# Kernel tuning notes

Hardware: AMD Instinct MI355X
Metric: run time of the kernel (lower is better)

The kernel has to match this reference:

```python
import jax, jax.numpy as jnp
import numpy as np

B, C, L = 32, 64, 2048
FREQ = L // 2 + 1            # 1025
BAND_SIZES = [341, 341, 343]  # freq//3, freq//3, remainder


def setup_inputs() -> dict:
    key = jax.random.key(0)
    k = jax.random.split(key, 6)
    X = jax.random.normal(k[0], (B, C, L), dtype=jnp.float32)
    A0 = jax.random.normal(k[1], (BAND_SIZES[0], BAND_SIZES[0]), dtype=jnp.float32)
    A1 = jax.random.normal(k[2], (BAND_SIZES[1], BAND_SIZES[1]), dtype=jnp.float32)
    A2 = jax.random.normal(k[3], (BAND_SIZES[2], BAND_SIZES[2]), dtype=jnp.float32)
    fusion_weights = jnp.ones((3,), dtype=jnp.float32)
    # Gumbel(0,1) noise for the 2-way gumbel-softmax over each (b, i, j) entry
    gumbel_noise = jax.random.gumbel(k[4], (B, C, C, 2), dtype=jnp.float32)
    return {"X": X, "A0": A0, "A1": A1, "A2": A2,
            "fusion_weights": fusion_weights, "gumbel_noise": gumbel_noise}


def _band_dist(band, A):
    # band: (b, c, s), A: (s, s). dist[b,i,j] = ||A (band_i - band_j)||^2
    # Gram trick: ||y_i - y_j||^2 = q_i + q_j - 2 y_i . y_j, y = band @ A^T
    Y = jnp.einsum('ds,bcs->bcd', A, band)          # (b, c, s)
    G = jnp.einsum('bid,bjd->bij', Y, Y)            # (b, c, c)
    q = jnp.einsum('bid,bid->bi', Y, Y)             # (b, c)
    dist = q[:, :, None] + q[:, None, :] - 2.0 * G
    return jnp.maximum(dist, 0.0)                   # guard fp round-off


def reference(X, A0, A1, A2, fusion_weights, gumbel_noise):
    XF = jnp.abs(jnp.fft.rfft(X, axis=-1))          # (b, c, FREQ)
    s0, s1, s2 = BAND_SIZES
    bands = (XF[..., :s0], XF[..., s0:s0 + s1], XF[..., s0 + s1:])
    As = (A0, A1, A2)
    dists = jnp.stack([_band_dist(b_, A_) for b_, A_ in zip(bands, As)], axis=-1)  # (b,c,c,3)
    w = jax.nn.softmax(fusion_weights)
    dist = jnp.einsum('bijk,k->bij', dists, w)      # (b, c, c)

    exp_dist = 1.0 / (dist + 1e-10)
    eye = jnp.eye(C, dtype=exp_dist.dtype)
    mask = 1.0 - eye
    exp_dist = exp_dist * mask
    exp_max = jax.lax.stop_gradient(jnp.max(exp_dist, axis=-1, keepdims=True))
    p = exp_dist / exp_max
    p = (p * mask + eye) * 0.99                     # probs in (0, 0.99]

    # Bernoulli via 2-class gumbel-softmax (hard, tau=1, straight-through)
    logits = jnp.stack([jnp.log(p / (1.0 - p)), jnp.log((1.0 - p) / p)], axis=-1)  # (b,c,c,2)
    y = logits + gumbel_noise
    y_soft = jax.nn.softmax(y, axis=-1)
    y_hard = jax.nn.one_hot(jnp.argmax(y, axis=-1), 2, dtype=y_soft.dtype)
    sample = (y_hard - jax.lax.stop_gradient(y_soft) + y_soft)[..., 0]  # (b,c,c)
    return sample[:, None, :, :]                    # (b, 1, c, c)
```

## Files before the change

kernel.cpp:

```cpp
#include <hip/hip_runtime.h>
#include <math.h>

#define Bn 32
#define Cn 64
#define Ln 2048
#define NFREQ 1025
#define S0c 341
#define S1c 341
#define S2c 343

#define PI_D 3.14159265358979323846

typedef double v4d __attribute__((ext_vector_type(4)));

#define PADIX(i) ((i) + ((i) >> 4))

__global__ void k_twiddle(double2* __restrict__ tw) {
    int t = blockIdx.x * blockDim.x + threadIdx.x;
    if (t < 2048) {
        double ang = -2.0 * PI_D * (double)t / 2048.0;
        double s, c;
        sincos(ang, &s, &c);
        tw[t] = make_double2(c, s);
    }
}

__device__ __forceinline__ int rev4_10(unsigned x) {
    unsigned t = __brev(x) >> 22;
    return (int)(((t & 0x155u) << 1) | ((t >> 1) & 0x155u));
}

__global__ __launch_bounds__(256) void k_fft(const float* __restrict__ X,
                                             const double2* __restrict__ tw,
                                             float* __restrict__ XF) {
    __shared__ double re[1088];
    __shared__ double im[1088];
    int row = blockIdx.x;
    int tid = threadIdx.x;
    const float2* xr = (const float2*)(X + (size_t)row * Ln);
    {
        int k = tid;
        float2 v0 = xr[k];
        float2 v1 = xr[k + 256];
        float2 v2 = xr[k + 512];
        float2 v3 = xr[k + 768];
        double ar = (double)v0.x, ai = (double)v0.y;
        double br = (double)v1.x, bi = (double)v1.y;
        double cr = (double)v2.x, ci = (double)v2.y;
        double dr = (double)v3.x, di = (double)v3.y;
        double2 w1 = tw[2 * k];
        double2 w2 = tw[4 * k];
        double2 w3 = tw[6 * k];
        double t0r = ar + cr, t0i = ai + ci;
        double t1r = ar - cr, t1i = ai - ci;
        double t2r = br + dr, t2i = bi + di;
        double t3r = br - dr, t3i = bi - di;
        int i0 = PADIX(k), i1 = PADIX(k + 256), i2 = PADIX(k + 512), i3 = PADIX(k + 768);
        re[i0] = t0r + t2r; im[i0] = t0i + t2i;
        double u1r = t1r + t3i, u1i = t1i - t3r;
        re[i1] = u1r * w1.x - u1i * w1.y; im[i1] = u1r * w1.y + u1i * w1.x;
        double u2r = t0r - t2r, u2i = t0i - t2i;
        re[i2] = u2r * w2.x - u2i * w2.y; im[i2] = u2r * w2.y + u2i * w2.x;
        double u3r = t1r - t3i, u3i = t1i + t3r;
        re[i3] = u3r * w3.x - u3i * w3.y; im[i3] = u3r * w3.y + u3i * w3.x;
    }
    __syncthreads();
    #pragma unroll
    for (int s = 1; s < 5; ++s) {
        int log2Q = 8 - 2 * s;
        int Q = 1 << log2Q;
        int k = tid & (Q - 1);
        int g = tid >> log2Q;
        int base = (g << (log2Q + 2)) + k;
        int i0 = PADIX(base), i1 = PADIX(base + Q), i2 = PADIX(base + 2 * Q), i3 = PADIX(base + 3 * Q);
        double ar = re[i0], ai = im[i0];
        double br = re[i1], bi = im[i1];
        double cr = re[i2], ci = im[i2];
        double dr = re[i3], di = im[i3];
        int step = 2 << (2 * s);
        double2 w1 = tw[k * step];
        double2 w2 = tw[2 * k * step];
        double2 w3 = tw[3 * k * step];
        double t0r = ar + cr, t0i = ai + ci;
        double t1r = ar - cr, t1i = ai - ci;
        double t2r = br + dr, t2i = bi + di;
        double t3r = br - dr, t3i = bi - di;
        re[i0] = t0r + t2r; im[i0] = t0i + t2i;
        double u1r = t1r + t3i, u1i = t1i - t3r;
        re[i1] = u1r * w1.x - u1i * w1.y; im[i1] = u1r * w1.y + u1i * w1.x;
        double u2r = t0r - t2r, u2i = t0i - t2i;
        re[i2] = u2r * w2.x - u2i * w2.y; im[i2] = u2r * w2.y + u2i * w2.x;
        double u3r = t1r - t3i, u3i = t1i + t3r;
        re[i3] = u3r * w3.x - u3i * w3.y; im[i3] = u3r * w3.y + u3i * w3.x;
        __syncthreads();
    }
    float* out = XF + (size_t)row * NFREQ;
    for (int k = tid; k <= 1024; k += 256) {
        double Xr, Xi;
        if (k == 0)        { Xr = re[0] + im[0]; Xi = 0.0; }
        else if (k == 1024){ Xr = re[0] - im[0]; Xi = 0.0; }
        else {
            int rv  = PADIX(rev4_10((unsigned)k));
            int rv2 = PADIX(rev4_10((unsigned)(1024 - k)));
            double Zr = re[rv],  Zi = im[rv];
            double Wr = re[rv2], Wi = im[rv2];
            double Er = 0.5 * (Zr + Wr), Ei = 0.5 * (Zi - Wi);
            double Or = 0.5 * (Zi + Wi), Oi = -0.5 * (Zr - Wr);
            double2 t = tw[k];
            Xr = Er + t.x * Or - t.y * Oi;
            Xi = Ei + t.x * Oi + t.y * Or;
        }
        out[k] = (float)sqrt(Xr * Xr + Xi * Xi);
    }
}

__global__ __launch_bounds__(256) void k_gemm(const float* __restrict__ XF,
                                              const float* __restrict__ A0,
                                              const float* __restrict__ A1,
                                              const float* __restrict__ A2,
                                              double* __restrict__ Y) {
    const int Sarr[3] = {S0c, S1c, S2c};
    const int Oarr[3] = {0, S0c, S0c + S1c};
    int bz = blockIdx.z;
    int z = bz >> 2, q = bz & 3;
    const float* A = (z == 0) ? A0 : ((z == 1) ? A1 : A2);
    int S = Sarr[z], O = Oarr[z];
    int qm = q >> 1, qn = q & 1;

    __shared__ float sX[32][66];
    __shared__ float sA[32][66];
    int r0 = blockIdx.x * 64 + qm * 32;
    int d0 = blockIdx.y * 64 + qn * 32;
    int tid = threadIdx.x;
    int lane = tid & 63, w = tid >> 6;
    int lm = (w >> 1) * 16, ln = (w & 1) * 16;
    int fm = lane & 15, kq = lane >> 4;
    int kl = tid & 63, rl = tid >> 6;

    v4d zero = {0.0, 0.0, 0.0, 0.0};
    double aval = (double)fm;
    v4d calR = __builtin_amdgcn_mfma_f64_16x16x4f64(aval, 1.0, zero, 0, 0, 0);
    v4d calC = __builtin_amdgcn_mfma_f64_16x16x4f64(1.0, aval, zero, 0, 0, 0);
    int rIdx[4], cIdx[4];
    #pragma unroll
    for (int i = 0; i < 4; ++i) {
        rIdx[i] = (int)(calR[i] * 0.25);
        cIdx[i] = (int)(calC[i] * 0.25);
    }

    auto load_tile = [&](int st, float* px, float* pa) {
        int ss = st * 64 + kl;
        bool sv = ss < S;
        #pragma unroll
        for (int i = 0; i < 8; ++i)
            px[i] = sv ? XF[(size_t)(r0 + rl + 4 * i) * NFREQ + O + ss] : 0.0f;
        #pragma unroll
        for (int j = 0; j < 8; ++j) {
            int d = d0 + rl + 4 * j;
            pa[j] = (sv && d < S) ? A[(size_t)d * S + ss] : 0.0f;
        }
    };

    v4d acc = zero;
    float px[8], pa[8];
    load_tile(0, px, pa);
    const int nsteps = 6;
    for (int st = 0; st < nsteps; ++st) {
        __syncthreads();
        #pragma unroll
        for (int i = 0; i < 8; ++i) sX[rl + 4 * i][kl] = px[i];
        #pragma unroll
        for (int j = 0; j < 8; ++j) sA[rl + 4 * j][kl] = pa[j];
        __syncthreads();
        if (st + 1 < nsteps) load_tile(st + 1, px, pa);
        #pragma unroll
        for (int t = 0; t < 16; ++t) {
            int k = 4 * t + kq;
            double a = (double)sX[lm + fm][k];
            double b = (double)sA[ln + fm][k];
            acc = __builtin_amdgcn_mfma_f64_16x16x4f64(a, b, acc, 0, 0, 0);
        }
    }
    #pragma unroll
    for (int i = 0; i < 4; ++i) {
        int row = r0 + lm + rIdx[i];
        int d = d0 + ln + cIdx[i];
        if (d < S) Y[(size_t)row * NFREQ + O + d] = acc[i];
    }
}

__global__ __launch_bounds__(256) void k_dist(const double* __restrict__ Y,
                                              const float* __restrict__ fw,
                                              double* __restrict__ part) {
    __shared__ double sY[64][34];
    int b = blockIdx.x;
    int chunk = blockIdx.y;
    int dlo = chunk * 128;
    int dhi = (chunk == 7) ? NFREQ : dlo + 128;
    int tid = threadIdx.x;
    int lane = tid & 63, w = tid >> 6;
    int wm = (w >> 1) * 32, wn = (w & 1) * 32;
    int fm = lane & 15, kq = lane >> 4;
    int kl = tid & 31, rl = tid >> 5;

    double f0 = (double)fw[0], f1 = (double)fw[1], f2 = (double)fw[2];
    double m = fmax(f0, fmax(f1, f2));
    double e0 = exp(f0 - m), e1 = exp(f1 - m), e2 = exp(f2 - m);
    double esum = e0 + e1 + e2;
    double sw0 = sqrt(e0 / esum), sw1 = sqrt(e1 / esum), sw2 = sqrt(e2 / esum);

    v4d zero = {0.0, 0.0, 0.0, 0.0};
    double aval = (double)fm;
    v4d calR = __builtin_amdgcn_mfma_f64_16x16x4f64(aval, 1.0, zero, 0, 0, 0);
    v4d calC = __builtin_amdgcn_mfma_f64_16x16x4f64(1.0, aval, zero, 0, 0, 0);
    int rIdx[4], cIdx[4];
    #pragma unroll
    for (int i = 0; i < 4; ++i) {
        rIdx[i] = (int)(calR[i] * 0.25);
        cIdx[i] = (int)(calC[i] * 0.25);
    }

    const double* Yb = Y + (size_t)b * Cn * NFREQ;
    auto load_tile = [&](int k0, double* py) {
        int d = dlo + k0 + kl;
        bool dv = d < dhi;
        double sw = dv ? ((d < S0c) ? sw0 : ((d < S0c + S1c) ? sw1 : sw2)) : 0.0;
        #pragma unroll
        for (int i = 0; i < 8; ++i)
            py[i] = dv ? Yb[(size_t)(rl + 8 * i) * NFREQ + d] * sw : 0.0;
    };

    v4d acc00 = zero, acc01 = zero, acc10 = zero, acc11 = zero;
    double py[8];
    load_tile(0, py);
    int nsteps = (dhi - dlo + 31) / 32;
    for (int st = 0; st < nsteps; ++st) {
        __syncthreads();
        #pragma unroll
        for (int i = 0; i < 8; ++i) sY[rl + 8 * i][kl] = py[i];
        __syncthreads();
        if (st + 1 < nsteps) load_tile((st + 1) * 32, py);
        #pragma unroll
        for (int t = 0; t < 8; ++t) {
            int k = 4 * t + kq;
            double a0 = sY[wm + fm][k];
            double a1 = sY[wm + 16 + fm][k];
            double b0 = sY[wn + fm][k];
            double b1 = sY[wn + 16 + fm][k];
            acc00 = __builtin_amdgcn_mfma_f64_16x16x4f64(a0, b0, acc00, 0, 0, 0);
            acc01 = __builtin_amdgcn_mfma_f64_16x16x4f64(a0, b1, acc01, 0, 0, 0);
            acc10 = __builtin_amdgcn_mfma_f64_16x16x4f64(a1, b0, acc10, 0, 0, 0);
            acc11 = __builtin_amdgcn_mfma_f64_16x16x4f64(a1, b1, acc11, 0, 0, 0);
        }
    }
    double* pb = part + (((size_t)b * 8 + chunk) << 12);
    #pragma unroll
    for (int i = 0; i < 4; ++i) {
        int rowA = wm + rIdx[i], rowB = rowA + 16;
        int cA = wn + cIdx[i], cB = cA + 16;
        pb[rowA * 64 + cA] = acc00[i];
        pb[rowA * 64 + cB] = acc01[i];
        pb[rowB * 64 + cA] = acc10[i];
        pb[rowB * 64 + cB] = acc11[i];
    }
}

__global__ __launch_bounds__(256) void k_decide(const double* __restrict__ part,
                                                const float* __restrict__ gum,
                                                float* __restrict__ out) {
    __shared__ double sQ[64];
    int b = blockIdx.x;
    int tid = threadIdx.x;
    const double* pb = part + (((size_t)b * 8) << 12);
    if (tid < 64) {
        double q = 0.0;
        #pragma unroll
        for (int c = 0; c < 8; ++c) q += pb[((size_t)c << 12) + tid * 65];
        sQ[tid] = q;
    }
    __syncthreads();
    int i = blockIdx.y * 4 + (tid >> 6);
    int j = tid & 63;
    double g = 0.0;
    #pragma unroll
    for (int c = 0; c < 8; ++c) g += pb[((size_t)c << 12) + i * 64 + j];
    double dist = fmax(sQ[i] + sQ[j] - 2.0 * g, 0.0);
    double e = (i == j) ? 0.0 : 1.0 / (dist + 1e-10);
    double emax = e;
    #pragma unroll
    for (int off = 32; off; off >>= 1)
        emax = fmax(emax, __shfl_xor(emax, off, 64));
    double p = (i == j) ? 0.99 : (e / emax) * 0.99;
    double l0 = log(p / (1.0 - p));
    double l1 = log((1.0 - p) / p);
    int idx = i * 64 + j;
    const float* gb = gum + (size_t)b * 8192;
    double y0 = l0 + (double)gb[2 * idx];
    double y1 = l1 + (double)gb[2 * idx + 1];
    out[(size_t)b * 4096 + idx] = (y0 >= y1) ? 1.0f : 0.0f;
}

extern "C" void kernel_launch(void* const* d_in, const int* in_sizes, int n_in,
                              void* d_out, int out_size, void* d_ws, size_t ws_size,
                              hipStream_t stream) {
    const float* X  = (const float*)d_in[0];
    const float* A0 = (const float*)d_in[1];
    const float* A1 = (const float*)d_in[2];
    const float* A2 = (const float*)d_in[3];
    const float* fw = (const float*)d_in[4];
    const float* gm = (const float*)d_in[5];
    float* out = (float*)d_out;

    char* ws = (char*)d_ws;
    double2* tw  = (double2*)(ws);
    float*   XF  = (float*)(ws + 32768);
    double*  Y   = (double*)(ws + 8429568);
    double*  part = (double*)(ws + 32768);

    k_twiddle<<<8, 256, 0, stream>>>(tw);
    k_fft<<<Bn * Cn, 256, 0, stream>>>(X, tw, XF);
    k_gemm<<<dim3(32, 6, 12), 256, 0, stream>>>(XF, A0, A1, A2, Y);
    k_dist<<<dim3(Bn, 8), 256, 0, stream>>>(Y, fw, part);
    k_decide<<<dim3(Bn, 16), 256, 0, stream>>>(part, gm, out);
}
```

Before: 161.8 us.

## Batch two FFT rows per block and shrink GEMM K-tile with dual accumulators

The FFT kernel now handles two rows per block, so twiddle loads and index math are shared across both rows and half as many blocks are launched. The GEMM kernel drops its K-tile from 64 to 32 and sizes the loop count per band (11 steps instead of a fixed 6×64), which removes padded zero work. It also splits the MFMA chain into two accumulators to break the dependency between successive MFMAs. In exchange the FFT uses twice the shared memory per block, the GEMM has more sync steps, and the FFT grid has fewer blocks.

```diff
diff --git a/kernel.cpp b/kernel.cpp
--- a/kernel.cpp
+++ b/kernel.cpp
@@ -33,36 +33,39 @@
 __global__ __launch_bounds__(256) void k_fft(const float* __restrict__ X,
                                              const double2* __restrict__ tw,
                                              float* __restrict__ XF) {
-    __shared__ double re[1088];
-    __shared__ double im[1088];
-    int row = blockIdx.x;
+    __shared__ double re[2][1088];
+    __shared__ double im[2][1088];
+    int row0 = blockIdx.x * 2;
     int tid = threadIdx.x;
-    const float2* xr = (const float2*)(X + (size_t)row * Ln);
     {
         int k = tid;
-        float2 v0 = xr[k];
-        float2 v1 = xr[k + 256];
-        float2 v2 = xr[k + 512];
-        float2 v3 = xr[k + 768];
-        double ar = (double)v0.x, ai = (double)v0.y;
-        double br = (double)v1.x, bi = (double)v1.y;
-        double cr = (double)v2.x, ci = (double)v2.y;
-        double dr = (double)v3.x, di = (double)v3.y;
         double2 w1 = tw[2 * k];
         double2 w2 = tw[4 * k];
         double2 w3 = tw[6 * k];
-        double t0r = ar + cr, t0i = ai + ci;
-        double t1r = ar - cr, t1i = ai - ci;
-        double t2r = br + dr, t2i = bi + di;
-        double t3r = br - dr, t3i = bi - di;
         int i0 = PADIX(k), i1 = PADIX(k + 256), i2 = PADIX(k + 512), i3 = PADIX(k + 768);
-        re[i0] = t0r + t2r; im[i0] = t0i + t2i;
-        double u1r = t1r + t3i, u1i = t1i - t3r;
-        re[i1] = u1r * w1.x - u1i * w1.y; im[i1] = u1r * w1.y + u1i * w1.x;
-        double u2r = t0r - t2r, u2i = t0i - t2i;
-        re[i2] = u2r * w2.x - u2i * w2.y; im[i2] = u2r * w2.y + u2i * w2.x;
-        double u3r = t1r - t3i, u3i = t1i + t3r;
-        re[i3] = u3r * w3.x - u3i * w3.y; im[i3] = u3r * w3.y + u3i * w3.x;
+        #pragma unroll
+        for (int r = 0; r < 2; ++r) {
+            const float2* xr = (const float2*)(X + (size_t)(row0 + r) * Ln);
+            float2 v0 = xr[k];
+            float2 v1 = xr[k + 256];
+            float2 v2 = xr[k + 512];
+            float2 v3 = xr[k + 768];
+            double ar = (double)v0.x, ai = (double)v0.y;
+            double br = (double)v1.x, bi = (double)v1.y;
+            double cr = (double)v2.x, ci = (double)v2.y;
+            double dr = (double)v3.x, di = (double)v3.y;
+            double t0r = ar + cr, t0i = ai + ci;
+            double t1r = ar - cr, t1i = ai - ci;
+            double t2r = br + dr, t2i = bi + di;
+            double t3r = br - dr, t3i = bi - di;
+            re[r][i0] = t0r + t2r; im[r][i0] = t0i + t2i;
+            double u1r = t1r + t3i, u1i = t1i - t3r;
+            re[r][i1] = u1r * w1.x - u1i * w1.y; im[r][i1] = u1r * w1.y + u1i * w1.x;
+            double u2r = t0r - t2r, u2i = t0i - t2i;
+            re[r][i2] = u2r * w2.x - u2i * w2.y; im[r][i2] = u2r * w2.y + u2i * w2.x;
+            double u3r = t1r - t3i, u3i = t1i + t3r;
+            re[r][i3] = u3r * w3.x - u3i * w3.y; im[r][i3] = u3r * w3.y + u3i * w3.x;
+        }
     }
     __syncthreads();
     #pragma unroll
@@ -73,44 +76,56 @@
         int g = tid >> log2Q;
         int base = (g << (log2Q + 2)) + k;
         int i0 = PADIX(base), i1 = PADIX(base + Q), i2 = PADIX(base + 2 * Q), i3 = PADIX(base + 3 * Q);
-        double ar = re[i0], ai = im[i0];
-        double br = re[i1], bi = im[i1];
-        double cr = re[i2], ci = im[i2];
-        double dr = re[i3], di = im[i3];
         int step = 2 << (2 * s);
         double2 w1 = tw[k * step];
         double2 w2 = tw[2 * k * step];
         double2 w3 = tw[3 * k * step];
-        double t0r = ar + cr, t0i = ai + ci;
-        double t1r = ar - cr, t1i = ai - ci;
-        double t2r = br + dr, t2i = bi + di;
-        double t3r = br - dr, t3i = bi - di;
-        re[i0] = t0r + t2r; im[i0] = t0i + t2i;
-        double u1r = t1r + t3i, u1i = t1i - t3r;
-        re[i1] = u1r * w1.x - u1i * w1.y; im[i1] = u1r * w1.y + u1i * w1.x;
-        double u2r = t0r - t2r, u2i = t0i - t2i;
-        re[i2] = u2r * w2.x - u2i * w2.y; im[i2] = u2r * w2.y + u2i * w2.x;
-        double u3r = t1r - t3i, u3i = t1i + t3r;
-        re[i3] = u3r * w3.x - u3i * w3.y; im[i3] = u3r * w3.y + u3i * w3.x;
-        __syncthreads();
-    }
-    float* out = XF + (size_t)row * NFREQ;
+        #pragma unroll
+        for (int r = 0; r < 2; ++r) {
+            double ar = re[r][i0], ai = im[r][i0];
+            double br = re[r][i1], bi = im[r][i1];
+            double cr = re[r][i2], ci = im[r][i2];
+            double dr = re[r][i3], di = im[r][i3];
+            double t0r = ar + cr, t0i = ai + ci;
+            double t1r = ar - cr, t1i = ai - ci;
+            double t2r = br + dr, t2i = bi + di;
+            double t3r = br - dr, t3i = bi - di;
+            re[r][i0] = t0r + t2r; im[r][i0] = t0i + t2i;
+            double u1r = t1r + t3i, u1i = t1i - t3r;
+            re[r][i1] = u1r * w1.x - u1i * w1.y; im[r][i1] = u1r * w1.y + u1i * w1.x;
+            double u2r = t0r - t2r, u2i = t0i - t2i;
+            re[r][i2] = u2r * w2.x - u2i * w2.y; im[r][i2] = u2r * w2.y + u2i * w2.x;
+            double u3r = t1r - t3i, u3i = t1i + t3r;
+            re[r][i3] = u3r * w3.x - u3i * w3.y; im[r][i3] = u3r * w3.y + u3i * w3.x;
+        }
+        __syncthreads();
+    }
+    float* out0 = XF + (size_t)row0 * NFREQ;
+    float* out1 = XF + (size_t)(row0 + 1) * NFREQ;
     for (int k = tid; k <= 1024; k += 256) {
-        double Xr, Xi;
-        if (k == 0)        { Xr = re[0] + im[0]; Xi = 0.0; }
-        else if (k == 1024){ Xr = re[0] - im[0]; Xi = 0.0; }
-        else {
-            int rv  = PADIX(rev4_10((unsigned)k));
-            int rv2 = PADIX(rev4_10((unsigned)(1024 - k)));
-            double Zr = re[rv],  Zi = im[rv];
-            double Wr = re[rv2], Wi = im[rv2];
-            double Er = 0.5 * (Zr + Wr), Ei = 0.5 * (Zi - Wi);
-            double Or = 0.5 * (Zi + Wi), Oi = -0.5 * (Zr - Wr);
-            double2 t = tw[k];
-            Xr = Er + t.x * Or - t.y * Oi;
-            Xi = Ei + t.x * Oi + t.y * Or;
-        }
-        out[k] = (float)sqrt(Xr * Xr + Xi * Xi);
+        int rv = 0, rv2 = 0;
+        double2 t = tw[0];
+        if (k != 0 && k != 1024) {
+            rv  = PADIX(rev4_10((unsigned)k));
+            rv2 = PADIX(rev4_10((unsigned)(1024 - k)));
+            t = tw[k];
+        }
+        #pragma unroll
+        for (int r = 0; r < 2; ++r) {
+            double Xr, Xi;
+            if (k == 0)        { Xr = re[r][0] + im[r][0]; Xi = 0.0; }
+            else if (k == 1024){ Xr = re[r][0] - im[r][0]; Xi = 0.0; }
+            else {
+                double Zr = re[r][rv],  Zi = im[r][rv];
+                double Wr = re[r][rv2], Wi = im[r][rv2];
+                double Er = 0.5 * (Zr + Wr), Ei = 0.5 * (Zi - Wi);
+                double Or = 0.5 * (Zi + Wi), Oi = -0.5 * (Zr - Wr);
+                Xr = Er + t.x * Or - t.y * Oi;
+                Xi = Ei + t.x * Oi + t.y * Or;
+            }
+            float v = (float)sqrt(Xr * Xr + Xi * Xi);
+            if (r == 0) out0[k] = v; else out1[k] = v;
+        }
     }
 }
 
@@ -127,15 +142,15 @@
     int S = Sarr[z], O = Oarr[z];
     int qm = q >> 1, qn = q & 1;
 
-    __shared__ float sX[32][66];
-    __shared__ float sA[32][66];
+    __shared__ float sX[32][34];
+    __shared__ float sA[32][34];
     int r0 = blockIdx.x * 64 + qm * 32;
     int d0 = blockIdx.y * 64 + qn * 32;
     int tid = threadIdx.x;
     int lane = tid & 63, w = tid >> 6;
     int lm = (w >> 1) * 16, ln = (w & 1) * 16;
     int fm = lane & 15, kq = lane >> 4;
-    int kl = tid & 63, rl = tid >> 6;
+    int kl = tid & 31, rl = tid >> 5;
 
     v4d zero = {0.0, 0.0, 0.0, 0.0};
     double aval = (double)fm;
@@ -149,38 +164,43 @@
     }
 
     auto load_tile = [&](int st, float* px, float* pa) {
-        int ss = st * 64 + kl;
+        int ss = st * 32 + kl;
         bool sv = ss < S;
         #pragma unroll
-        for (int i = 0; i < 8; ++i)
-            px[i] = sv ? XF[(size_t)(r0 + rl + 4 * i) * NFREQ + O + ss] : 0.0f;
-        #pragma unroll
-        for (int j = 0; j < 8; ++j) {
-            int d = d0 + rl + 4 * j;
+        for (int i = 0; i < 4; ++i)
+            px[i] = sv ? XF[(size_t)(r0 + rl + 8 * i) * NFREQ + O + ss] : 0.0f;
+        #pragma unroll
+        for (int j = 0; j < 4; ++j) {
+            int d = d0 + rl + 8 * j;
             pa[j] = (sv && d < S) ? A[(size_t)d * S + ss] : 0.0f;
         }
     };
 
-    v4d acc = zero;
-    float px[8], pa[8];
+    v4d accE = zero, accO = zero;
+    float px[4], pa[4];
     load_tile(0, px, pa);
-    const int nsteps = 6;
+    int nsteps = (S + 31) / 32;
     for (int st = 0; st < nsteps; ++st) {
         __syncthreads();
         #pragma unroll
-        for (int i = 0; i < 8; ++i) sX[rl + 4 * i][kl] = px[i];
-        #pragma unroll
-        for (int j = 0; j < 8; ++j) sA[rl + 4 * j][kl] = pa[j];
+        for (int i = 0; i < 4; ++i) sX[rl + 8 * i][kl] = px[i];
+        #pragma unroll
+        for (int j = 0; j < 4; ++j) sA[rl + 8 * j][kl] = pa[j];
         __syncthreads();
         if (st + 1 < nsteps) load_tile(st + 1, px, pa);
         #pragma unroll
-        for (int t = 0; t < 16; ++t) {
-            int k = 4 * t + kq;
-            double a = (double)sX[lm + fm][k];
-            double b = (double)sA[ln + fm][k];
-            acc = __builtin_amdgcn_mfma_f64_16x16x4f64(a, b, acc, 0, 0, 0);
-        }
-    }
+        for (int t = 0; t < 4; ++t) {
+            int kE = 8 * t + kq;
+            int kO = 8 * t + 4 + kq;
+            double aE = (double)sX[lm + fm][kE];
+            double bE = (double)sA[ln + fm][kE];
+            double aO = (double)sX[lm + fm][kO];
+            double bO = (double)sA[ln + fm][kO];
+            accE = __builtin_amdgcn_mfma_f64_16x16x4f64(aE, bE, accE, 0, 0, 0);
+            accO = __builtin_amdgcn_mfma_f64_16x16x4f64(aO, bO, accO, 0, 0, 0);
+        }
+    }
+    v4d acc = accE + accO;
     #pragma unroll
     for (int i = 0; i < 4; ++i) {
         int row = r0 + lm + rIdx[i];
@@ -318,7 +338,7 @@
     double*  part = (double*)(ws + 32768);
 
     k_twiddle<<<8, 256, 0, stream>>>(tw);
-    k_fft<<<Bn * Cn, 256, 0, stream>>>(X, tw, XF);
+    k_fft<<<Bn * Cn / 2, 256, 0, stream>>>(X, tw, XF);
     k_gemm<<<dim3(32, 6, 12), 256, 0, stream>>>(XF, A0, A1, A2, Y);
     k_dist<<<dim3(Bn, 8), 256, 0, stream>>>(Y, fw, part);
     k_decide<<<dim3(Bn, 16), 256, 0, stream>>>(part, gm, out);
```

New measurement: 165.0 us. About the same (+2.0%).
